# Performance work log

Measured on AMD Instinct MI355X. Metric: run time of the kernel, lower is better.

## Reference

```python
import jax, jax.numpy as jnp
import numpy as np

GROUPS = 32
EPS = 1e-5


def group_norm(x, gamma, beta):
    # x: [B, C, H, W]; normalize over (C//G, H, W) within each of G groups
    B, C, H, W = x.shape
    xg = x.reshape(B, GROUPS, C // GROUPS, H, W)
    mean = xg.mean(axis=(2, 3, 4), keepdims=True)
    var = xg.var(axis=(2, 3, 4), keepdims=True)
    xg = (xg - mean) * jax.lax.rsqrt(var + EPS)
    x = xg.reshape(B, C, H, W)
    return x * gamma[None, :, None, None] + beta[None, :, None, None]


def conv1x1(x, W, b):
    # 1x1 conv == pointwise linear over channels. x: [B,C,H,W], W: [Cout,Cin]
    return jnp.einsum('oc,bchw->bohw', W, x) + b[None, :, None, None]


def setup_inputs() -> dict:
    key = jax.random.key(0)
    ks = jax.random.split(key, 6)
    B, C, H, W = 16, 512, 32, 32
    scale = 1.0 / np.sqrt(C)  # ~kaiming-ish init for 1x1 convs
    return {
        'x': jax.random.normal(ks[0], (B, C, H, W), jnp.float32),
        'gn_gamma': jnp.ones((C,), jnp.float32),
        'gn_beta': jnp.zeros((C,), jnp.float32),
        'Wq': jax.random.normal(ks[1], (C, C), jnp.float32) * scale,
        'bq': jnp.zeros((C,), jnp.float32),
        'Wk': jax.random.normal(ks[2], (C, C), jnp.float32) * scale,
        'bk': jnp.zeros((C,), jnp.float32),
        'Wv': jax.random.normal(ks[3], (C, C), jnp.float32) * scale,
        'bv': jnp.zeros((C,), jnp.float32),
        'Wp': jax.random.normal(ks[4], (C, C), jnp.float32) * scale,
        'bp': jnp.zeros((C,), jnp.float32),
    }


def reference(x, gn_gamma, gn_beta, Wq, bq, Wk, bk, Wv, bv, Wp, bp):
    B, C, H, W = x.shape
    h = group_norm(x, gn_gamma, gn_beta)
    q = conv1x1(h, Wq, bq).reshape(B, C, H * W)  # [B,C,T]
    k = conv1x1(h, Wk, bk).reshape(B, C, H * W)
    v = conv1x1(h, Wv, bv).reshape(B, C, H * W)
    # scores [B, T(query), S(key)] = q^T k, scaled by C^{-1/2}
    w = jnp.einsum('bct,bcs->bts', q, k) * (C ** -0.5)
    w = jax.nn.softmax(w, axis=-1)
    h = jnp.einsum('bts,bcs->bct', w, v).reshape(B, C, H, W)
    h = conv1x1(h, Wp, bp)
    return x + h
```

## Files before the change

kernel.cpp:

```cpp
#include <hip/hip_runtime.h>

typedef unsigned short u16;
typedef __bf16 bf16x8 __attribute__((ext_vector_type(8)));
typedef float f32x16 __attribute__((ext_vector_type(16)));

__device__ __forceinline__ u16 f2bf(float f) {
    unsigned u = __builtin_bit_cast(unsigned, f);
    u += 0x7fffu + ((u >> 16) & 1u);
    return (u16)(u >> 16);
}
__device__ __forceinline__ float bf2f(u16 h) {
    return __builtin_bit_cast(float, (unsigned)h << 16);
}

#define GLDS16(g, l) __builtin_amdgcn_global_load_lds( \
    (const __attribute__((address_space(1))) void*)(g), \
    (__attribute__((address_space(3))) void*)(l), 16, 0, 0)

#define QK_SCALE 0.044194173824159216f

__global__ __launch_bounds__(256) void convert_kernel(
    const float* __restrict__ Wq, const float* __restrict__ Wk,
    const float* __restrict__ Wv, const float* __restrict__ Wp,
    const float* __restrict__ bq, const float* __restrict__ bk,
    const float* __restrict__ bv,
    u16* __restrict__ Wqkv, u16* __restrict__ Wpb, float* __restrict__ bqkv)
{
    int idx = blockIdx.x * 256 + threadIdx.x;
    if (idx < 786432) {
        int which = idx >> 18;
        int off   = idx & 262143;
        if (which == 0)
            Wqkv[idx] = f2bf(Wq[off] * QK_SCALE);
        else
            Wqkv[idx] = f2bf(((which == 1) ? Wk : Wv)[off]);
    } else {
        int off = idx - 786432;
        Wpb[off] = f2bf(Wp[off]);
    }
    if (idx < 1536) {
        float bvv = (idx < 512) ? bq[idx] * QK_SCALE
                  : (idx < 1024) ? bk[idx & 511] : bv[idx & 511];
        bqkv[idx] = bvv;
    }
}

__global__ __launch_bounds__(256) void gn_kernel(
    const float* __restrict__ x, const float* __restrict__ gamma,
    const float* __restrict__ beta, u16* __restrict__ ht)
{
    const int g = blockIdx.x, b = blockIdx.y, tid = threadIdx.x;
    const float* xg = x + ((size_t)b * 512 + (size_t)g * 16) * 1024;

    float s = 0.f, s2 = 0.f;
    const float4* x4 = (const float4*)xg;
    #pragma unroll 4
    for (int i = tid; i < 4096; i += 256) {
        float4 v = x4[i];
        s  += v.x + v.y + v.z + v.w;
        s2 += v.x * v.x + v.y * v.y + v.z * v.z + v.w * v.w;
    }
    #pragma unroll
    for (int off = 32; off; off >>= 1) {
        s  += __shfl_down(s, off);
        s2 += __shfl_down(s2, off);
    }
    __shared__ float rs[4], rs2[4];
    __shared__ float stat[2];
    const int w = tid >> 6;
    if ((tid & 63) == 0) { rs[w] = s; rs2[w] = s2; }
    __syncthreads();
    if (tid == 0) {
        float S  = rs[0] + rs[1] + rs[2] + rs[3];
        float S2 = rs2[0] + rs2[1] + rs2[2] + rs2[3];
        float mean = S * (1.f / 16384.f);
        float var  = S2 * (1.f / 16384.f) - mean * mean;
        stat[0] = mean;
        stat[1] = rsqrtf(var + 1e-5f);
    }
    __syncthreads();
    const float mean = stat[0], rstd = stat[1];

    float ga[16], be[16];
    #pragma unroll
    for (int ci = 0; ci < 16; ci++) {
        ga[ci] = gamma[g * 16 + ci];
        be[ci] = beta[g * 16 + ci];
    }
    for (int t = tid; t < 1024; t += 256) {
        u16 yv[16];
        #pragma unroll
        for (int ci = 0; ci < 16; ci++) {
            float v = xg[ci * 1024 + t];
            yv[ci] = f2bf((v - mean) * rstd * ga[ci] + be[ci]);
        }
        uint4* dst = (uint4*)(ht + ((size_t)b * 1024 + t) * 512 + g * 16);
        dst[0] = ((const uint4*)yv)[0];
        dst[1] = ((const uint4*)yv)[1];
    }
}

__global__ __launch_bounds__(256) void softmax_kernel(u16* __restrict__ scores)
{
    const int row  = blockIdx.x * 4 + (threadIdx.x >> 6);
    const int lane = threadIdx.x & 63;
    u16* p = scores + (size_t)row * 1024 + lane * 16;

    uint4 w0 = ((const uint4*)p)[0];
    uint4 w1 = ((const uint4*)p)[1];
    unsigned wd[8] = {w0.x, w0.y, w0.z, w0.w, w1.x, w1.y, w1.z, w1.w};
    float v[16];
    #pragma unroll
    for (int i = 0; i < 8; i++) {
        v[2 * i]     = __builtin_bit_cast(float, wd[i] << 16);
        v[2 * i + 1] = __builtin_bit_cast(float, wd[i] & 0xffff0000u);
    }
    float m = v[0];
    #pragma unroll
    for (int i = 1; i < 16; i++) m = fmaxf(m, v[i]);
    #pragma unroll
    for (int off = 1; off < 64; off <<= 1) m = fmaxf(m, __shfl_xor(m, off));

    float s = 0.f;
    #pragma unroll
    for (int i = 0; i < 16; i++) { v[i] = __expf(v[i] - m); s += v[i]; }
    #pragma unroll
    for (int off = 1; off < 64; off <<= 1) s += __shfl_xor(s, off);
    const float inv = 1.0f / s;

    #pragma unroll
    for (int i = 0; i < 8; i++) {
        unsigned lo = f2bf(v[2 * i] * inv);
        unsigned hi = f2bf(v[2 * i + 1] * inv);
        wd[i] = lo | (hi << 16);
    }
    ((uint4*)p)[0] = make_uint4(wd[0], wd[1], wd[2], wd[3]);
    ((uint4*)p)[1] = make_uint4(wd[4], wd[5], wd[6], wd[7]);
}

template <int MODE>
__global__ __launch_bounds__(256) void gemm_nt(
    const u16* __restrict__ A, const u16* __restrict__ B,
    size_t strideA, size_t strideB, int lda, int ldb, int K,
    u16* __restrict__ o0, u16* __restrict__ o1, u16* __restrict__ o2,
    float* __restrict__ fo, const float* __restrict__ bias,
    const float* __restrict__ xres)
{
    __shared__ u16 As[128 * 64];
    __shared__ u16 Bs[128 * 64];

    const int tid   = threadIdx.x;
    const int lane  = tid & 63;
    const int wave  = tid >> 6;
    const int wm    = (wave >> 1) * 64;
    const int wn    = (wave & 1) * 64;
    const int l31   = lane & 31;
    const int khalf = lane >> 5;
    const int b     = blockIdx.z;

    const u16* Ab = A + (size_t)b * strideA + (size_t)blockIdx.y * 128 * lda;
    const u16* Bb = B + (size_t)b * strideB + (size_t)blockIdx.x * 128 * ldb;

    const int srow = lane >> 3;
    const int sc   = lane & 7;
    const int scg  = sc ^ srow;

    f32x16 acc[2][2] = {};

    for (int k0 = 0; k0 < K; k0 += 64) {
        __syncthreads();
        #pragma unroll
        for (int s = 0; s < 4; s++) {
            const int r = wave * 32 + s * 8 + srow;
            GLDS16(Ab + (size_t)r * lda + k0 + scg * 8, As + r * 64 + sc * 8);
            GLDS16(Bb + (size_t)r * ldb + k0 + scg * 8, Bs + r * 64 + sc * 8);
        }
        __syncthreads();

        #pragma unroll
        for (int ks = 0; ks < 4; ks++) {
            const int cidx = ks * 2 + khalf;
            const int slot = (cidx ^ (lane & 7)) * 8;
            bf16x8 af[2], bfr[2];
            #pragma unroll
            for (int i = 0; i < 2; i++)
                af[i] = *(const bf16x8*)(As + (wm + i * 32 + l31) * 64 + slot);
            #pragma unroll
            for (int j = 0; j < 2; j++)
                bfr[j] = *(const bf16x8*)(Bs + (wn + j * 32 + l31) * 64 + slot);
            #pragma unroll
            for (int i = 0; i < 2; i++)
                #pragma unroll
                for (int j = 0; j < 2; j++)
                    acc[i][j] = __builtin_amdgcn_mfma_f32_32x32x16_bf16(
                        af[i], bfr[j], acc[i][j], 0, 0, 0);
        }
    }

    const int m_base = blockIdx.y * 128 + wm + 4 * khalf;
    const int n_base = blockIdx.x * 128 + wn + l31;

    #pragma unroll
    for (int i = 0; i < 2; i++) {
        #pragma unroll
        for (int j = 0; j < 2; j++) {
            const int n = n_base + j * 32;
            float bv = 0.f;
            if (MODE == 0 || MODE == 3) bv = bias[n];
            #pragma unroll
            for (int g = 0; g < 4; g++) {
                const int m = m_base + i * 32 + 8 * g;
                const float a0 = acc[i][j][4 * g]     + bv;
                const float a1 = acc[i][j][4 * g + 1] + bv;
                const float a2 = acc[i][j][4 * g + 2] + bv;
                const float a3 = acc[i][j][4 * g + 3] + bv;
                if (MODE == 0) {
                    if (n < 1024) {
                        u16* dst = (n < 512) ? o0 : o1;
                        const int nn = n & 511;
                        dst[((size_t)b * 1024 + m) * 512 + nn]     = f2bf(a0);
                        dst[((size_t)b * 1024 + m + 1) * 512 + nn] = f2bf(a1);
                        dst[((size_t)b * 1024 + m + 2) * 512 + nn] = f2bf(a2);
                        dst[((size_t)b * 1024 + m + 3) * 512 + nn] = f2bf(a3);
                    } else {
                        ushort4 hv = {f2bf(a0), f2bf(a1), f2bf(a2), f2bf(a3)};
                        *(ushort4*)(o2 + ((size_t)b * 512 + (n - 1024)) * 1024 + m) = hv;
                    }
                } else if (MODE == 1) {
                    ushort4 hv = {f2bf(a0), f2bf(a1), f2bf(a2), f2bf(a3)};
                    *(ushort4*)(o0 + ((size_t)b * 1024 + n) * 1024 + m) = hv;
                } else if (MODE == 2) {
                    ushort4 hv = {f2bf(a0), f2bf(a1), f2bf(a2), f2bf(a3)};
                    *(ushort4*)(o0 + ((size_t)b * 1024 + n) * 512 + m) = hv;
                } else {
                    const size_t off = ((size_t)b * 512 + n) * 1024 + m;
                    const float4 xv = *(const float4*)(xres + off);
                    float4 ov = {a0 + xv.x, a1 + xv.y, a2 + xv.z, a3 + xv.w};
                    *(float4*)(fo + off) = ov;
                }
            }
        }
    }
}

extern "C" void kernel_launch(void* const* d_in, const int* in_sizes, int n_in,
                              void* d_out, int out_size, void* d_ws, size_t ws_size,
                              hipStream_t stream)
{
    const float* x     = (const float*)d_in[0];
    const float* gamma = (const float*)d_in[1];
    const float* beta  = (const float*)d_in[2];
    const float* Wq    = (const float*)d_in[3];
    const float* bq    = (const float*)d_in[4];
    const float* Wk    = (const float*)d_in[5];
    const float* bk    = (const float*)d_in[6];
    const float* Wv    = (const float*)d_in[7];
    const float* bv    = (const float*)d_in[8];
    const float* Wp    = (const float*)d_in[9];
    const float* bp    = (const float*)d_in[10];

    char* ws = (char*)d_ws;
    u16*   Wqkv   = (u16*)(ws + 0);
    u16*   Wpb    = (u16*)(ws + 1572864);
    float* bqkv   = (float*)(ws + 2097152);
    u16*   ht     = (u16*)(ws + 2105344);
    u16*   kt     = (u16*)(ws + 18882560);
    u16*   vv     = (u16*)(ws + 35659776);
    u16*   scores = (u16*)(ws + 52436992);
    u16*   qt  = (u16*)d_out;
    u16*   h2  = ht;
    float* out = (float*)d_out;

    convert_kernel<<<4096, 256, 0, stream>>>(Wq, Wk, Wv, Wp, bq, bk, bv,
                                             Wqkv, Wpb, bqkv);
    gn_kernel<<<dim3(32, 16), 256, 0, stream>>>(x, gamma, beta, ht);

    gemm_nt<0><<<dim3(12, 8, 16), 256, 0, stream>>>(
        ht, Wqkv, 524288, 0, 512, 512, 512,
        qt, kt, vv, nullptr, bqkv, nullptr);

    gemm_nt<1><<<dim3(8, 8, 16), 256, 0, stream>>>(
        kt, qt, 524288, 524288, 512, 512, 512,
        scores, nullptr, nullptr, nullptr, nullptr, nullptr);

    softmax_kernel<<<4096, 256, 0, stream>>>(scores);

    gemm_nt<2><<<dim3(8, 4, 16), 256, 0, stream>>>(
        vv, scores, 524288, 1048576, 1024, 1024, 1024,
        h2, nullptr, nullptr, nullptr, nullptr, nullptr);

    gemm_nt<3><<<dim3(4, 8, 16), 256, 0, stream>>>(
        h2, Wpb, 524288, 0, 512, 512, 512,
        nullptr, nullptr, nullptr, out, bp, x);
}
```

Before: 258.0 us.

## Pre-swizzle B operands into MFMA fragment layout and load directly to registers

The B operands (weights, Q, softmax scores) are now written in a fragment-major layout that matches the 32x32x16 MFMA register layout. Each wave can then load its B fragments straight from global memory into registers, with no LDS staging. The A tile grows to 256 rows in LDS with a new XOR swizzle, and each wave computes a 128x64 output. The convert, QKV-projection epilogue, scores epilogue and softmax indexing are all rewritten for the new layouts. This removes B's LDS traffic and one shared buffer, at the cost of uncoalesced per-wave global B loads, higher register pressure, and halved grid sizes.

```diff
diff --git a/kernel.cpp b/kernel.cpp
--- a/kernel.cpp
+++ b/kernel.cpp
@@ -9,15 +9,13 @@
     u += 0x7fffu + ((u >> 16) & 1u);
     return (u16)(u >> 16);
 }
-__device__ __forceinline__ float bf2f(u16 h) {
-    return __builtin_bit_cast(float, (unsigned)h << 16);
-}
 
 #define GLDS16(g, l) __builtin_amdgcn_global_load_lds( \
     (const __attribute__((address_space(1))) void*)(g), \
     (__attribute__((address_space(3))) void*)(l), 16, 0, 0)
 
 #define QK_SCALE 0.044194173824159216f
+
 
 __global__ __launch_bounds__(256) void convert_kernel(
     const float* __restrict__ Wq, const float* __restrict__ Wk,
@@ -26,22 +24,39 @@
     const float* __restrict__ bv,
     u16* __restrict__ Wqkv, u16* __restrict__ Wpb, float* __restrict__ bqkv)
 {
-    int idx = blockIdx.x * 256 + threadIdx.x;
-    if (idx < 786432) {
-        int which = idx >> 18;
-        int off   = idx & 262143;
-        if (which == 0)
-            Wqkv[idx] = f2bf(Wq[off] * QK_SCALE);
-        else
-            Wqkv[idx] = f2bf(((which == 1) ? Wk : Wv)[off]);
+    const int t = blockIdx.x * 256 + threadIdx.x;
+    const float* W;
+    u16* dst;
+    int n, k;
+    float sc = 1.0f;
+    if (t < 98304) {
+        const int nb = t >> 11, rem = t & 2047;
+        const int kb = rem >> 6, ln = rem & 63;
+        n = nb * 32 + (ln & 31);
+        k = kb * 16 + (ln >> 5) * 8;
+        if (n < 512)       { W = Wq; sc = QK_SCALE; }
+        else if (n < 1024) { W = Wk; n -= 512; }
+        else               { W = Wv; n -= 1024; }
+        dst = Wqkv + (size_t)t * 8;
     } else {
-        int off = idx - 786432;
-        Wpb[off] = f2bf(Wp[off]);
-    }
-    if (idx < 1536) {
-        float bvv = (idx < 512) ? bq[idx] * QK_SCALE
-                  : (idx < 1024) ? bk[idx & 511] : bv[idx & 511];
-        bqkv[idx] = bvv;
+        const int t2 = t - 98304;
+        const int nb = t2 >> 11, rem = t2 & 2047;
+        const int kb = rem >> 6, ln = rem & 63;
+        n = nb * 32 + (ln & 31);
+        k = kb * 16 + (ln >> 5) * 8;
+        W = Wp;
+        dst = Wpb + (size_t)t2 * 8;
+    }
+    const float4 f0 = *(const float4*)(W + (size_t)n * 512 + k);
+    const float4 f1 = *(const float4*)(W + (size_t)n * 512 + k + 4);
+    u16 o[8] = {f2bf(f0.x * sc), f2bf(f0.y * sc), f2bf(f0.z * sc), f2bf(f0.w * sc),
+                f2bf(f1.x * sc), f2bf(f1.y * sc), f2bf(f1.z * sc), f2bf(f1.w * sc)};
+    *(uint4*)dst = *(const uint4*)o;
+
+    if (t < 1536) {
+        float bvv = (t < 512) ? bq[t] * QK_SCALE
+                  : (t < 1024) ? bk[t & 511] : bv[t & 511];
+        bqkv[t] = bvv;
     }
 }
 
@@ -104,10 +119,12 @@
 {
     const int row  = blockIdx.x * 4 + (threadIdx.x >> 6);
     const int lane = threadIdx.x & 63;
-    u16* p = scores + (size_t)row * 1024 + lane * 16;
-
-    uint4 w0 = ((const uint4*)p)[0];
-    uint4 w1 = ((const uint4*)p)[1];
+    const int b = row >> 10, t = row & 1023;
+    u16* p = scores + (size_t)b * 1048576 +
+             ((size_t)(t >> 5) * 64 + lane) * 512 + (t & 31) * 8;
+
+    uint4 w0 = *(const uint4*)p;
+    uint4 w1 = *(const uint4*)(p + 256);
     unsigned wd[8] = {w0.x, w0.y, w0.z, w0.w, w1.x, w1.y, w1.z, w1.w};
     float v[16];
     #pragma unroll
@@ -134,106 +151,123 @@
         unsigned hi = f2bf(v[2 * i + 1] * inv);
         wd[i] = lo | (hi << 16);
     }
-    ((uint4*)p)[0] = make_uint4(wd[0], wd[1], wd[2], wd[3]);
-    ((uint4*)p)[1] = make_uint4(wd[4], wd[5], wd[6], wd[7]);
+    *(uint4*)p         = make_uint4(wd[0], wd[1], wd[2], wd[3]);
+    *(uint4*)(p + 256) = make_uint4(wd[4], wd[5], wd[6], wd[7]);
 }
 
 template <int MODE>
-__global__ __launch_bounds__(256) void gemm_nt(
+__global__ __launch_bounds__(256, 2) void gemm_flat(
     const u16* __restrict__ A, const u16* __restrict__ B,
-    size_t strideA, size_t strideB, int lda, int ldb, int K,
+    size_t strideA, size_t strideB, int lda, int Kd16, int K,
     u16* __restrict__ o0, u16* __restrict__ o1, u16* __restrict__ o2,
     float* __restrict__ fo, const float* __restrict__ bias,
     const float* __restrict__ xres)
 {
-    __shared__ u16 As[128 * 64];
-    __shared__ u16 Bs[128 * 64];
+    __shared__ u16 As[256 * 64];
 
     const int tid   = threadIdx.x;
     const int lane  = tid & 63;
     const int wave  = tid >> 6;
-    const int wm    = (wave >> 1) * 64;
+    const int wm    = (wave >> 1) * 128;
     const int wn    = (wave & 1) * 64;
     const int l31   = lane & 31;
     const int khalf = lane >> 5;
     const int b     = blockIdx.z;
 
-    const u16* Ab = A + (size_t)b * strideA + (size_t)blockIdx.y * 128 * lda;
-    const u16* Bb = B + (size_t)b * strideB + (size_t)blockIdx.x * 128 * ldb;
+    const u16* Ab = A + (size_t)b * strideA + (size_t)blockIdx.y * 256 * lda;
+    const u16* Bb = B + (size_t)b * strideB;
+    const int nb0 = blockIdx.x * 4 + (wave & 1) * 2;
 
     const int srow = lane >> 3;
     const int sc   = lane & 7;
-    const int scg  = sc ^ srow;
-
-    f32x16 acc[2][2] = {};
+    const int rkey = (l31 & 7) ^ ((l31 >> 2) & 7);
+
+    f32x16 acc[4][2] = {};
 
     for (int k0 = 0; k0 < K; k0 += 64) {
+        const int kb16 = k0 >> 4;
         __syncthreads();
-        #pragma unroll
-        for (int s = 0; s < 4; s++) {
-            const int r = wave * 32 + s * 8 + srow;
-            GLDS16(Ab + (size_t)r * lda + k0 + scg * 8, As + r * 64 + sc * 8);
-            GLDS16(Bb + (size_t)r * ldb + k0 + scg * 8, Bs + r * 64 + sc * 8);
+        bf16x8 breg[4][2];
+        #pragma unroll
+        for (int kb = 0; kb < 4; kb++)
+            #pragma unroll
+            for (int j = 0; j < 2; j++)
+                breg[kb][j] = *(const bf16x8*)(
+                    Bb + ((size_t)(nb0 + j) * Kd16 + kb16 + kb) * 512 + lane * 8);
+        #pragma unroll
+        for (int s = 0; s < 8; s++) {
+            const int r = wave * 64 + s * 8 + srow;
+            const int key = srow ^ ((2 * s + khalf) & 7);
+            GLDS16(Ab + (size_t)r * lda + k0 + (sc ^ key) * 8,
+                   As + r * 64 + sc * 8);
         }
         __syncthreads();
 
         #pragma unroll
-        for (int ks = 0; ks < 4; ks++) {
-            const int cidx = ks * 2 + khalf;
-            const int slot = (cidx ^ (lane & 7)) * 8;
-            bf16x8 af[2], bfr[2];
+        for (int kb = 0; kb < 4; kb++) {
+            const int slot = ((kb * 2 + khalf) ^ rkey) * 8;
+            bf16x8 af[4];
             #pragma unroll
-            for (int i = 0; i < 2; i++)
+            for (int i = 0; i < 4; i++)
                 af[i] = *(const bf16x8*)(As + (wm + i * 32 + l31) * 64 + slot);
             #pragma unroll
-            for (int j = 0; j < 2; j++)
-                bfr[j] = *(const bf16x8*)(Bs + (wn + j * 32 + l31) * 64 + slot);
-            #pragma unroll
-            for (int i = 0; i < 2; i++)
+            for (int i = 0; i < 4; i++)
                 #pragma unroll
                 for (int j = 0; j < 2; j++)
                     acc[i][j] = __builtin_amdgcn_mfma_f32_32x32x16_bf16(
-                        af[i], bfr[j], acc[i][j], 0, 0, 0);
+                        af[i], breg[kb][j], acc[i][j], 0, 0, 0);
         }
     }
 
-    const int m_base = blockIdx.y * 128 + wm + 4 * khalf;
-    const int n_base = blockIdx.x * 128 + wn + l31;
-
-    #pragma unroll
-    for (int i = 0; i < 2; i++) {
+    const int mb = blockIdx.y * 256 + wm;
+    const int nbase = blockIdx.x * 128 + wn + l31;
+
+    #pragma unroll
+    for (int i = 0; i < 4; i++) {
         #pragma unroll
         for (int j = 0; j < 2; j++) {
-            const int n = n_base + j * 32;
+            const int n = nbase + j * 32;
             float bv = 0.f;
             if (MODE == 0 || MODE == 3) bv = bias[n];
             #pragma unroll
             for (int g = 0; g < 4; g++) {
-                const int m = m_base + i * 32 + 8 * g;
+                const int m0 = mb + i * 32 + 4 * khalf + 8 * g;
                 const float a0 = acc[i][j][4 * g]     + bv;
                 const float a1 = acc[i][j][4 * g + 1] + bv;
                 const float a2 = acc[i][j][4 * g + 2] + bv;
                 const float a3 = acc[i][j][4 * g + 3] + bv;
                 if (MODE == 0) {
-                    if (n < 1024) {
-                        u16* dst = (n < 512) ? o0 : o1;
-                        const int nn = n & 511;
-                        dst[((size_t)b * 1024 + m) * 512 + nn]     = f2bf(a0);
-                        dst[((size_t)b * 1024 + m + 1) * 512 + nn] = f2bf(a1);
-                        dst[((size_t)b * 1024 + m + 2) * 512 + nn] = f2bf(a2);
-                        dst[((size_t)b * 1024 + m + 3) * 512 + nn] = f2bf(a3);
+                    if (n < 512) {
+                        const int c = n;
+                        u16* qp = o0 + (size_t)b * 524288 +
+                            ((size_t)((m0 >> 5)) * 32 + (c >> 4)) * 512 +
+                            ((m0 & 31) + ((c >> 3) & 1) * 32) * 8 + (c & 7);
+                        qp[0]  = f2bf(a0);
+                        qp[8]  = f2bf(a1);
+                        qp[16] = f2bf(a2);
+                        qp[24] = f2bf(a3);
+                    } else if (n < 1024) {
+                        const int c = n - 512;
+                        u16* kp = o1 + ((size_t)b * 1024 + m0) * 512 + c;
+                        kp[0]    = f2bf(a0);
+                        kp[512]  = f2bf(a1);
+                        kp[1024] = f2bf(a2);
+                        kp[1536] = f2bf(a3);
                     } else {
                         ushort4 hv = {f2bf(a0), f2bf(a1), f2bf(a2), f2bf(a3)};
-                        *(ushort4*)(o2 + ((size_t)b * 512 + (n - 1024)) * 1024 + m) = hv;
+                        *(ushort4*)(o2 + ((size_t)b * 512 + (n - 1024)) * 1024 + m0) = hv;
                     }
                 } else if (MODE == 1) {
                     ushort4 hv = {f2bf(a0), f2bf(a1), f2bf(a2), f2bf(a3)};
-                    *(ushort4*)(o0 + ((size_t)b * 1024 + n) * 1024 + m) = hv;
+                    u16* pp = o0 + (size_t)b * 1048576 +
+                        ((size_t)(n >> 5) * 64 + (m0 >> 4)) * 512 +
+                        ((n & 31) + (g & 1) * 32) * 8 + 4 * khalf;
+                    *(ushort4*)pp = hv;
                 } else if (MODE == 2) {
                     ushort4 hv = {f2bf(a0), f2bf(a1), f2bf(a2), f2bf(a3)};
-                    *(ushort4*)(o0 + ((size_t)b * 1024 + n) * 512 + m) = hv;
+                    *(ushort4*)(o0 + ((size_t)b * 1024 + n) * 512 + m0) = hv;
                 } else {
-                    const size_t off = ((size_t)b * 512 + n) * 1024 + m;
+                    const size_t off = ((size_t)b * 512 + n) * 1024 + m0;
                     const float4 xv = *(const float4*)(xres + off);
                     float4 ov = {a0 + xv.x, a1 + xv.y, a2 + xv.z, a3 + xv.w};
                     *(float4*)(fo + off) = ov;
@@ -271,25 +305,25 @@
     u16*   h2  = ht;
     float* out = (float*)d_out;
 
-    convert_kernel<<<4096, 256, 0, stream>>>(Wq, Wk, Wv, Wp, bq, bk, bv,
-                                             Wqkv, Wpb, bqkv);
+    convert_kernel<<<512, 256, 0, stream>>>(Wq, Wk, Wv, Wp, bq, bk, bv,
+                                            Wqkv, Wpb, bqkv);
     gn_kernel<<<dim3(32, 16), 256, 0, stream>>>(x, gamma, beta, ht);
 
-    gemm_nt<0><<<dim3(12, 8, 16), 256, 0, stream>>>(
-        ht, Wqkv, 524288, 0, 512, 512, 512,
+    gemm_flat<0><<<dim3(12, 4, 16), 256, 0, stream>>>(
+        ht, Wqkv, 524288, 0, 512, 32, 512,
         qt, kt, vv, nullptr, bqkv, nullptr);
 
-    gemm_nt<1><<<dim3(8, 8, 16), 256, 0, stream>>>(
-        kt, qt, 524288, 524288, 512, 512, 512,
+    gemm_flat<1><<<dim3(8, 4, 16), 256, 0, stream>>>(
+        kt, qt, 524288, 524288, 512, 32, 512,
         scores, nullptr, nullptr, nullptr, nullptr, nullptr);
 
     softmax_kernel<<<4096, 256, 0, stream>>>(scores);
 
-    gemm_nt<2><<<dim3(8, 4, 16), 256, 0, stream>>>(
-        vv, scores, 524288, 1048576, 1024, 1024, 1024,
+    gemm_flat<2><<<dim3(8, 2, 16), 256, 0, stream>>>(
+        vv, scores, 524288, 1048576, 1024, 64, 1024,
         h2, nullptr, nullptr, nullptr, nullptr, nullptr);
 
-    gemm_nt<3><<<dim3(4, 8, 16), 256, 0, stream>>>(
-        h2, Wpb, 524288, 0, 512, 512, 512,
+    gemm_flat<3><<<dim3(4, 4, 16), 256, 0, stream>>>(
+        h2, Wpb, 524288, 0, 512, 32, 512,
         nullptr, nullptr, nullptr, out, bp, x);
 }
```

Result: slower. 271.6 us (+5.3%).

## Fuse QK^T, softmax and PV into a flash-attention kernel

Applied to the files above, without the earlier changes.

Replaces the score GEMM, the standalone softmax and the PV GEMM with one kernel that keeps 64 queries per block, streams K and V in tiles, and applies an online softmax with running max and sum rescaling. This avoids writing and re-reading the full bf16 score matrix and removes two kernel launches. The fused kernel launches only 256 blocks with no double buffering and several block-wide barriers per tile, so occupancy and latency hiding may suffer. The gemm LDS read swizzle is also changed to key on the row index rather than the lane.

```diff
diff --git a/kernel.cpp b/kernel.cpp
--- a/kernel.cpp
+++ b/kernel.cpp
@@ -9,13 +9,13 @@
     u += 0x7fffu + ((u >> 16) & 1u);
     return (u16)(u >> 16);
 }
-__device__ __forceinline__ float bf2f(u16 h) {
-    return __builtin_bit_cast(float, (unsigned)h << 16);
-}
 
 #define GLDS16(g, l) __builtin_amdgcn_global_load_lds( \
     (const __attribute__((address_space(1))) void*)(g), \
     (__attribute__((address_space(3))) void*)(l), 16, 0, 0)
+
+#define WAIT_VM0()   asm volatile("s_waitcnt vmcnt(0)" ::: "memory")
+#define WAIT_ALL0()  asm volatile("s_waitcnt vmcnt(0) lgkmcnt(0)" ::: "memory")
 
 #define QK_SCALE 0.044194173824159216f
 
@@ -100,44 +100,6 @@
     }
 }
 
-__global__ __launch_bounds__(256) void softmax_kernel(u16* __restrict__ scores)
-{
-    const int row  = blockIdx.x * 4 + (threadIdx.x >> 6);
-    const int lane = threadIdx.x & 63;
-    u16* p = scores + (size_t)row * 1024 + lane * 16;
-
-    uint4 w0 = ((const uint4*)p)[0];
-    uint4 w1 = ((const uint4*)p)[1];
-    unsigned wd[8] = {w0.x, w0.y, w0.z, w0.w, w1.x, w1.y, w1.z, w1.w};
-    float v[16];
-    #pragma unroll
-    for (int i = 0; i < 8; i++) {
-        v[2 * i]     = __builtin_bit_cast(float, wd[i] << 16);
-        v[2 * i + 1] = __builtin_bit_cast(float, wd[i] & 0xffff0000u);
-    }
-    float m = v[0];
-    #pragma unroll
-    for (int i = 1; i < 16; i++) m = fmaxf(m, v[i]);
-    #pragma unroll
-    for (int off = 1; off < 64; off <<= 1) m = fmaxf(m, __shfl_xor(m, off));
-
-    float s = 0.f;
-    #pragma unroll
-    for (int i = 0; i < 16; i++) { v[i] = __expf(v[i] - m); s += v[i]; }
-    #pragma unroll
-    for (int off = 1; off < 64; off <<= 1) s += __shfl_xor(s, off);
-    const float inv = 1.0f / s;
-
-    #pragma unroll
-    for (int i = 0; i < 8; i++) {
-        unsigned lo = f2bf(v[2 * i] * inv);
-        unsigned hi = f2bf(v[2 * i + 1] * inv);
-        wd[i] = lo | (hi << 16);
-    }
-    ((uint4*)p)[0] = make_uint4(wd[0], wd[1], wd[2], wd[3]);
-    ((uint4*)p)[1] = make_uint4(wd[4], wd[5], wd[6], wd[7]);
-}
-
 template <int MODE>
 __global__ __launch_bounds__(256) void gemm_nt(
     const u16* __restrict__ A, const u16* __restrict__ B,
@@ -180,14 +142,17 @@
         #pragma unroll
         for (int ks = 0; ks < 4; ks++) {
             const int cidx = ks * 2 + khalf;
-            const int slot = (cidx ^ (lane & 7)) * 8;
             bf16x8 af[2], bfr[2];
             #pragma unroll
-            for (int i = 0; i < 2; i++)
-                af[i] = *(const bf16x8*)(As + (wm + i * 32 + l31) * 64 + slot);
-            #pragma unroll
-            for (int j = 0; j < 2; j++)
-                bfr[j] = *(const bf16x8*)(Bs + (wn + j * 32 + l31) * 64 + slot);
+            for (int i = 0; i < 2; i++) {
+                const int r = wm + i * 32 + l31;
+                af[i] = *(const bf16x8*)(As + r * 64 + ((cidx ^ (r & 7)) * 8));
+            }
+            #pragma unroll
+            for (int j = 0; j < 2; j++) {
+                const int r = wn + j * 32 + l31;
+                bfr[j] = *(const bf16x8*)(Bs + r * 64 + ((cidx ^ (r & 7)) * 8));
+            }
             #pragma unroll
             for (int i = 0; i < 2; i++)
                 #pragma unroll
@@ -226,12 +191,6 @@
                         ushort4 hv = {f2bf(a0), f2bf(a1), f2bf(a2), f2bf(a3)};
                         *(ushort4*)(o2 + ((size_t)b * 512 + (n - 1024)) * 1024 + m) = hv;
                     }
-                } else if (MODE == 1) {
-                    ushort4 hv = {f2bf(a0), f2bf(a1), f2bf(a2), f2bf(a3)};
-                    *(ushort4*)(o0 + ((size_t)b * 1024 + n) * 1024 + m) = hv;
-                } else if (MODE == 2) {
-                    ushort4 hv = {f2bf(a0), f2bf(a1), f2bf(a2), f2bf(a3)};
-                    *(ushort4*)(o0 + ((size_t)b * 1024 + n) * 512 + m) = hv;
                 } else {
                     const size_t off = ((size_t)b * 512 + n) * 1024 + m;
                     const float4 xv = *(const float4*)(xres + off);
@@ -241,6 +200,211 @@
             }
         }
     }
+}
+
+__global__ __launch_bounds__(256, 2) void attn_fused(
+    const u16* __restrict__ q, const u16* __restrict__ k,
+    const u16* __restrict__ v, u16* __restrict__ o)
+{
+    __shared__ u16 shA[16384];
+    __shared__ u16 shB[16384];
+    float* statf = (float*)shA;
+
+    const int tid  = threadIdx.x;
+    const int lane = tid & 63, w = tid >> 6;
+    const int l31  = lane & 31, kh = lane >> 5;
+    const int b = blockIdx.y, t0 = blockIdx.x * 64;
+
+    const u16* qb = q + (size_t)b * 524288 + (size_t)t0 * 512;
+    const u16* kb = k + (size_t)b * 524288;
+    const u16* vb = v + (size_t)b * 524288;
+
+    const int srow8  = lane >> 3, sc8 = lane & 7;
+    const int srow16 = lane >> 2, sc4 = lane & 3;
+
+    f32x16 oacc[2][4] = {};
+    float m_run[2] = {-3e38f, -3e38f};
+    float l_run[2] = {0.f, 0.f};
+
+    for (int s0 = 0; s0 < 1024; s0 += 256) {
+        f32x16 sacc[2][2] = {};
+        for (int k0 = 0; k0 < 512; k0 += 64) {
+            WAIT_ALL0();
+            #pragma unroll
+            for (int g = 0; g < 8; g++) {
+                const int r = w * 64 + g * 8 + srow8;
+                GLDS16(kb + (size_t)(s0 + r) * 512 + k0 + ((sc8 ^ (r & 7)) * 8),
+                       shA + r * 64 + sc8 * 8);
+            }
+            #pragma unroll
+            for (int g = 0; g < 8; g++) {
+                const int r = g * 8 + srow8;
+                GLDS16(qb + (size_t)r * 512 + k0 + ((sc8 ^ (r & 7)) * 8),
+                       shB + w * 4096 + r * 64 + sc8 * 8);
+            }
+            WAIT_VM0();
+            #pragma unroll
+            for (int ks = 0; ks < 4; ks++) {
+                const int cidx = ks * 2 + kh;
+                bf16x8 af[2], bq2[2];
+                #pragma unroll
+                for (int i = 0; i < 2; i++) {
+                    const int r = w * 64 + i * 32 + l31;
+                    af[i] = *(const bf16x8*)(shA + r * 64 + ((cidx ^ (r & 7)) * 8));
+                }
+                #pragma unroll
+                for (int j = 0; j < 2; j++) {
+                    const int r = j * 32 + l31;
+                    bq2[j] = *(const bf16x8*)(shB + w * 4096 + r * 64 +
+                                              ((cidx ^ (r & 7)) * 8));
+                }
+                #pragma unroll
+                for (int i = 0; i < 2; i++)
+                    #pragma unroll
+                    for (int j = 0; j < 2; j++)
+                        sacc[i][j] = __builtin_amdgcn_mfma_f32_32x32x16_bf16(
+                            af[i], bq2[j], sacc[i][j], 0, 0, 0);
+            }
+        }
+        __syncthreads();
+        float tm[2], al[2];
+        #pragma unroll
+        for (int j = 0; j < 2; j++) {
+            float m = sacc[0][j][0];
+            #pragma unroll
+            for (int r = 1; r < 16; r++) m = fmaxf(m, sacc[0][j][r]);
+            #pragma unroll
+            for (int r = 0; r < 16; r++) m = fmaxf(m, sacc[1][j][r]);
+            m = fmaxf(m, __shfl_xor(m, 32));
+            tm[j] = m;
+        }
+        if (kh == 0) {
+            statf[w * 64 + l31]      = tm[0];
+            statf[w * 64 + 32 + l31] = tm[1];
+        }
+        __syncthreads();
+        #pragma unroll
+        for (int j = 0; j < 2; j++) {
+            const int tj = j * 32 + l31;
+            float M = statf[tj];
+            #pragma unroll
+            for (int wi = 1; wi < 4; wi++) M = fmaxf(M, statf[wi * 64 + tj]);
+            const float m_new = fmaxf(m_run[j], M);
+            al[j] = __expf(m_run[j] - m_new);
+            m_run[j] = m_new;
+            float ls = 0.f;
+            #pragma unroll
+            for (int i = 0; i < 2; i++)
+                #pragma unroll
+                for (int r = 0; r < 16; r++) {
+                    float p = __expf(sacc[i][j][r] - m_new);
+                    sacc[i][j][r] = p;
+                    ls += p;
+                }
+            ls += __shfl_xor(ls, 32);
+            if (kh == 0) statf[256 + w * 64 + tj] = ls;
+        }
+        if (w == 0 && kh == 0) {
+            statf[512 + l31]      = al[0];
+            statf[512 + 32 + l31] = al[1];
+        }
+        #pragma unroll
+        for (int i = 0; i < 2; i++)
+            #pragma unroll
+            for (int j = 0; j < 2; j++) {
+                const int t = j * 32 + l31;
+                #pragma unroll
+                for (int g = 0; g < 4; g++) {
+                    const int c = w * 8 + i * 4 + g;
+                    u16 p4[4] = {f2bf(sacc[i][j][4*g]),   f2bf(sacc[i][j][4*g+1]),
+                                 f2bf(sacc[i][j][4*g+2]), f2bf(sacc[i][j][4*g+3])};
+                    *(uint2*)(shB + t * 256 + ((c ^ (t & 7)) * 8) + kh * 4) =
+                        *(const uint2*)p4;
+                }
+            }
+        __syncthreads();
+        #pragma unroll
+        for (int j = 0; j < 2; j++) {
+            const int tj = j * 32 + l31;
+            float L = statf[256 + tj];
+            #pragma unroll
+            for (int wi = 1; wi < 4; wi++) L += statf[256 + wi * 64 + tj];
+            l_run[j] = l_run[j] * al[j] + L;
+        }
+        #pragma unroll
+        for (int i = 0; i < 2; i++)
+            #pragma unroll
+            for (int g = 0; g < 4; g++) {
+                const int tq = i * 32 + 4 * kh + 8 * g;
+                const float4 av = *(const float4*)(statf + 512 + tq);
+                #pragma unroll
+                for (int j = 0; j < 4; j++) {
+                    oacc[i][j][4*g]   *= av.x;
+                    oacc[i][j][4*g+1] *= av.y;
+                    oacc[i][j][4*g+2] *= av.z;
+                    oacc[i][j][4*g+3] *= av.w;
+                }
+            }
+        __syncthreads();
+        for (int sv = 0; sv < 256; sv += 32) {
+            WAIT_ALL0();
+            #pragma unroll
+            for (int g = 0; g < 8; g++) {
+                const int r = w * 128 + g * 16 + srow16;
+                GLDS16(vb + (size_t)r * 1024 + s0 + sv +
+                           ((sc4 ^ ((r >> 1) & 3)) * 8),
+                       shA + r * 32 + sc4 * 8);
+            }
+            WAIT_VM0();
+            #pragma unroll
+            for (int ks = 0; ks < 2; ks++) {
+                bf16x8 pf[2], vf[4];
+                const int cbase = (sv >> 3) + ks * 2 + kh;
+                #pragma unroll
+                for (int i = 0; i < 2; i++) {
+                    const int t = i * 32 + l31;
+                    pf[i] = *(const bf16x8*)(shB + t * 256 +
+                                             ((cbase ^ (t & 7)) * 8));
+                }
+                #pragma unroll
+                for (int j = 0; j < 4; j++) {
+                    const int cr = w * 128 + j * 32 + l31;
+                    const int c4 = ks * 2 + kh;
+                    vf[j] = *(const bf16x8*)(shA + cr * 32 +
+                                             ((c4 ^ ((cr >> 1) & 3)) * 8));
+                }
+                #pragma unroll
+                for (int i = 0; i < 2; i++)
+                    #pragma unroll
+                    for (int j = 0; j < 4; j++)
+                        oacc[i][j] = __builtin_amdgcn_mfma_f32_32x32x16_bf16(
+                            pf[i], vf[j], oacc[i][j], 0, 0, 0);
+            }
+        }
+        __syncthreads();
+    }
+    if (w == 0 && kh == 0) {
+        statf[512 + l31]      = 1.0f / l_run[0];
+        statf[512 + 32 + l31] = 1.0f / l_run[1];
+    }
+    __syncthreads();
+    u16* ob = o + (size_t)b * 524288 + (size_t)t0 * 512;
+    #pragma unroll
+    for (int i = 0; i < 2; i++)
+        #pragma unroll
+        for (int g = 0; g < 4; g++) {
+            const int tq = i * 32 + 4 * kh + 8 * g;
+            const float4 lv = *(const float4*)(statf + 512 + tq);
+            #pragma unroll
+            for (int j = 0; j < 4; j++) {
+                const int c = w * 128 + j * 32 + l31;
+                u16* dst = ob + (size_t)tq * 512 + c;
+                dst[0]    = f2bf(oacc[i][j][4*g]   * lv.x);
+                dst[512]  = f2bf(oacc[i][j][4*g+1] * lv.y);
+                dst[1024] = f2bf(oacc[i][j][4*g+2] * lv.z);
+                dst[1536] = f2bf(oacc[i][j][4*g+3] * lv.w);
+            }
+        }
 }
 
 extern "C" void kernel_launch(void* const* d_in, const int* in_sizes, int n_in,
@@ -266,7 +430,6 @@
     u16*   ht     = (u16*)(ws + 2105344);
     u16*   kt     = (u16*)(ws + 18882560);
     u16*   vv     = (u16*)(ws + 35659776);
-    u16*   scores = (u16*)(ws + 52436992);
     u16*   qt  = (u16*)d_out;
     u16*   h2  = ht;
     float* out = (float*)d_out;
@@ -279,15 +442,7 @@
         ht, Wqkv, 524288, 0, 512, 512, 512,
         qt, kt, vv, nullptr, bqkv, nullptr);
 
-    gemm_nt<1><<<dim3(8, 8, 16), 256, 0, stream>>>(
-        kt, qt, 524288, 524288, 512, 512, 512,
-        scores, nullptr, nullptr, nullptr, nullptr, nullptr);
-
-    softmax_kernel<<<4096, 256, 0, stream>>>(scores);
-
-    gemm_nt<2><<<dim3(8, 4, 16), 256, 0, stream>>>(
-        vv, scores, 524288, 1048576, 1024, 1024, 1024,
-        h2, nullptr, nullptr, nullptr, nullptr, nullptr);
+    attn_fused<<<dim3(16, 16), 256, 0, stream>>>(qt, kt, vv, h2);
 
     gemm_nt<3><<<dim3(4, 8, 16), 256, 0, stream>>>(
         h2, Wpb, 524288, 0, 512, 512, 512,
```

New measurement: 364.4 us. 41.2% more time.

## Double-buffer LDS tiles in bf16 GEMM with async prefetch and new swizzle

Applied to the files above, without the earlier changes.

The GEMM main loop now uses two LDS buffers per operand. It issues the global-to-LDS loads for the next K tile before computing on the current one, so memory latency overlaps with MFMA work, and it uses explicit vmcnt waits and raw s_barrier. The XOR swizzle key also changes to a pattern that depends on the row, aimed at reducing LDS bank conflicts on the fragment reads. LDS use per block doubles, which may reduce occupancy, and the hand-written waitcnt and barrier logic has to be correct.

```diff
diff --git a/kernel.cpp b/kernel.cpp
--- a/kernel.cpp
+++ b/kernel.cpp
@@ -9,13 +9,13 @@
     u += 0x7fffu + ((u >> 16) & 1u);
     return (u16)(u >> 16);
 }
-__device__ __forceinline__ float bf2f(u16 h) {
-    return __builtin_bit_cast(float, (unsigned)h << 16);
-}
 
 #define GLDS16(g, l) __builtin_amdgcn_global_load_lds( \
     (const __attribute__((address_space(1))) void*)(g), \
     (__attribute__((address_space(3))) void*)(l), 16, 0, 0)
+
+#define BAR()       asm volatile("s_barrier" ::: "memory")
+#define WAITVM(n)   asm volatile("s_waitcnt vmcnt(" #n ")" ::: "memory")
 
 #define QK_SCALE 0.044194173824159216f
 
@@ -146,8 +146,8 @@
     float* __restrict__ fo, const float* __restrict__ bias,
     const float* __restrict__ xres)
 {
-    __shared__ u16 As[128 * 64];
-    __shared__ u16 Bs[128 * 64];
+    __shared__ u16 As[2][8192];
+    __shared__ u16 Bs[2][8192];
 
     const int tid   = threadIdx.x;
     const int lane  = tid & 63;
@@ -163,31 +163,48 @@
 
     const int srow = lane >> 3;
     const int sc   = lane & 7;
-    const int scg  = sc ^ srow;
+    const int rkey = (l31 & 7) ^ ((l31 >> 2) & 7);
 
     f32x16 acc[2][2] = {};
 
+    #pragma unroll
+    for (int s = 0; s < 4; s++) {
+        const int r   = wave * 32 + s * 8 + srow;
+        const int key = srow ^ ((2 * s + (srow >> 2)) & 7);
+        GLDS16(Ab + (size_t)r * lda + ((sc ^ key) * 8), As[0] + r * 64 + sc * 8);
+        GLDS16(Bb + (size_t)r * ldb + ((sc ^ key) * 8), Bs[0] + r * 64 + sc * 8);
+    }
+
+    int cur = 0;
     for (int k0 = 0; k0 < K; k0 += 64) {
-        __syncthreads();
-        #pragma unroll
-        for (int s = 0; s < 4; s++) {
-            const int r = wave * 32 + s * 8 + srow;
-            GLDS16(Ab + (size_t)r * lda + k0 + scg * 8, As + r * 64 + sc * 8);
-            GLDS16(Bb + (size_t)r * ldb + k0 + scg * 8, Bs + r * 64 + sc * 8);
+        if (k0 + 64 < K) {
+            const int nb = cur ^ 1;
+            const int kn = k0 + 64;
+            #pragma unroll
+            for (int s = 0; s < 4; s++) {
+                const int r   = wave * 32 + s * 8 + srow;
+                const int key = srow ^ ((2 * s + (srow >> 2)) & 7);
+                GLDS16(Ab + (size_t)r * lda + kn + ((sc ^ key) * 8),
+                       As[nb] + r * 64 + sc * 8);
+                GLDS16(Bb + (size_t)r * ldb + kn + ((sc ^ key) * 8),
+                       Bs[nb] + r * 64 + sc * 8);
+            }
+            WAITVM(8);
+        } else {
+            WAITVM(0);
         }
-        __syncthreads();
+        BAR();
 
         #pragma unroll
         for (int ks = 0; ks < 4; ks++) {
-            const int cidx = ks * 2 + khalf;
-            const int slot = (cidx ^ (lane & 7)) * 8;
+            const int slot = ((ks * 2 + khalf) ^ rkey) * 8;
             bf16x8 af[2], bfr[2];
             #pragma unroll
             for (int i = 0; i < 2; i++)
-                af[i] = *(const bf16x8*)(As + (wm + i * 32 + l31) * 64 + slot);
+                af[i] = *(const bf16x8*)(As[cur] + (wm + i * 32 + l31) * 64 + slot);
             #pragma unroll
             for (int j = 0; j < 2; j++)
-                bfr[j] = *(const bf16x8*)(Bs + (wn + j * 32 + l31) * 64 + slot);
+                bfr[j] = *(const bf16x8*)(Bs[cur] + (wn + j * 32 + l31) * 64 + slot);
             #pragma unroll
             for (int i = 0; i < 2; i++)
                 #pragma unroll
@@ -195,6 +212,8 @@
                     acc[i][j] = __builtin_amdgcn_mfma_f32_32x32x16_bf16(
                         af[i], bfr[j], acc[i][j], 0, 0, 0);
         }
+        BAR();
+        cur ^= 1;
     }
 
     const int m_base = blockIdx.y * 128 + wm + 4 * khalf;
```

Result: no change. 259.0 us (+0.4%).
